# Performance work log

Measured on AMD Instinct MI355X. Metric: run time of the kernel, lower is better.

The kernel has to match this reference:

```python
import jax, jax.numpy as jnp
import numpy as np

B, S, D, H = 2, 2048, 1024, 16
DK = D // H


def setup_inputs() -> dict:
    key = jax.random.key(0)
    ks = jax.random.split(key, 12)
    sc = 1.0 / np.sqrt(D)
    inp = {
        'q': jax.random.normal(ks[0], (B, S, D), jnp.float32),
        'k': jax.random.normal(ks[1], (B, S, D), jnp.float32),
        'v': jax.random.normal(ks[2], (B, S, D), jnp.float32),
        'mask': jnp.tril(jnp.ones((S, S), jnp.int32))[None, None],  # causal [1,1,S,S]
        'w_q': jax.random.normal(ks[3], (D, D), jnp.float32) * sc,
        'b_q': jnp.zeros((D,), jnp.float32),
        'w_k': jax.random.normal(ks[4], (D, D), jnp.float32) * sc,
        'b_k': jnp.zeros((D,), jnp.float32),
        'w_v': jax.random.normal(ks[5], (D, D), jnp.float32) * sc,
        'b_v': jnp.zeros((D,), jnp.float32),
        'w_o': jax.random.normal(ks[6], (D, D), jnp.float32) * sc,
        'b_o': jnp.zeros((D,), jnp.float32),
    }
    return inp


def _split_heads(x):
    # [B,S,D] -> [B,H,S,DK]
    b, s, _ = x.shape
    return x.reshape(b, s, H, DK).transpose(0, 2, 1, 3)


def reference(q, k, v, mask, w_q, b_q, w_k, b_k, w_v, b_v, w_o, b_o):
    # Linear projections (torch Linear: x @ W.T + b)
    qh = _split_heads(q @ w_q.T + b_q)
    kh = _split_heads(k @ w_k.T + b_k)
    vh = _split_heads(v @ w_v.T + b_v)
    scores = jnp.einsum('bhqd,bhkd->bhqk', qh, kh) / jnp.sqrt(jnp.float32(DK))
    scores = jnp.where(mask == 0, jnp.float32(-1e9), scores)
    probs = jax.nn.softmax(scores, axis=-1)
    # dropout is identity in eval mode
    ctx = jnp.einsum('bhqk,bhkd->bhqd', probs, vh)  # [B,H,S,DK]
    ctx = ctx.transpose(0, 2, 1, 3).reshape(q.shape[0], -1, D)
    out = ctx @ w_o.T + b_o
    return out, probs
```

## Files before the change

### kernel.cpp

```cpp
#include <hip/hip_runtime.h>

typedef float f32x4 __attribute__((ext_vector_type(4)));
typedef short s16x8 __attribute__((ext_vector_type(8)));
typedef short s16x4 __attribute__((ext_vector_type(4)));

#define MFMA(a, b, c) __builtin_amdgcn_mfma_f32_16x16x32_bf16((a), (b), (c), 0, 0, 0)

static __device__ __forceinline__ short f2bf(float f) {
  union { float ff; unsigned u; } v; v.ff = f;
  unsigned r = v.u + 0x7FFFu + ((v.u >> 16) & 1u);
  return (short)(r >> 16);
}

typedef __attribute__((address_space(3))) void lds_void_t;
typedef const __attribute__((address_space(1))) void gmem_void_t;
static __device__ __forceinline__ void gload_lds16(const void* g, void* l) {
  __builtin_amdgcn_global_load_lds((gmem_void_t*)g, (lds_void_t*)l, 16, 0, 0);
}

__global__ __launch_bounds__(256) void cvt_qkv_kernel(
    const float* __restrict__ q, const float* __restrict__ k, const float* __restrict__ v,
    short* __restrict__ qo, short* __restrict__ ko, short* __restrict__ vo) {
  const int y = blockIdx.y;
  const float* s = (y == 0) ? q : (y == 1) ? k : v;
  short* d = (y == 0) ? qo : (y == 1) ? ko : vo;
  const int i = blockIdx.x * 256 + threadIdx.x;
  const f32x4* s4 = (const f32x4*)s;
  f32x4 a = s4[2 * i], b = s4[2 * i + 1];
  s16x8 o;
  o[0] = f2bf(a[0]); o[1] = f2bf(a[1]); o[2] = f2bf(a[2]); o[3] = f2bf(a[3]);
  o[4] = f2bf(b[0]); o[5] = f2bf(b[1]); o[6] = f2bf(b[2]); o[7] = f2bf(b[3]);
  ((s16x8*)d)[i] = o;
}

__global__ __launch_bounds__(256) void cvt_w_kernel(
    const float* __restrict__ w0, const float* __restrict__ w1,
    const float* __restrict__ w2, const float* __restrict__ w3,
    short* __restrict__ o0, short* __restrict__ o1,
    short* __restrict__ o2, short* __restrict__ o3) {
  const int y = blockIdx.y;
  const float* s = (y == 0) ? w0 : (y == 1) ? w1 : (y == 2) ? w2 : w3;
  short* d = (y == 0) ? o0 : (y == 1) ? o1 : (y == 2) ? o2 : o3;
  const int i = blockIdx.x * 256 + threadIdx.x;
  const f32x4* s4 = (const f32x4*)s;
  f32x4 a = s4[2 * i], b = s4[2 * i + 1];
  s16x8 o;
  o[0] = f2bf(a[0]); o[1] = f2bf(a[1]); o[2] = f2bf(a[2]); o[3] = f2bf(a[3]);
  o[4] = f2bf(b[0]); o[5] = f2bf(b[1]); o[6] = f2bf(b[2]); o[7] = f2bf(b[3]);
  ((s16x8*)d)[i] = o;
}

template <int MODE, int NFRAG>
static __device__ __forceinline__ void gemm_body(
    const short* __restrict__ A, const short* __restrict__ Bt,
    const float* __restrict__ bias, void* __restrict__ outp) {
  constexpr int BN = NFRAG * 32;
  __shared__ short As[4096];
  __shared__ short Bs[BN * 32];
  const int t = threadIdx.x;
  const int lane = t & 63, wave = t >> 6;
  const int wr = wave >> 1, wc = wave & 1;
  const int lr = lane & 15, lg = lane >> 4;
  const int mBase = blockIdx.x * 128, nBase = blockIdx.y * BN;

  const int rowA = t >> 2, kcA = (t & 3) << 3;
  const short* gA = A + (size_t)(mBase + rowA) * 1024 + kcA;
  const short* gB = Bt + (size_t)(nBase + rowA) * 1024 + kcA;

  f32x4 acc[4][NFRAG] = {};

  for (int k0 = 0; k0 < 1024; k0 += 32) {
    __syncthreads();
    gload_lds16(gA + k0, &As[t * 8]);
    gload_lds16(gA + 64 * 1024 + k0, &As[2048 + t * 8]);
    gload_lds16(gB + k0, &Bs[t * 8]);
    if constexpr (NFRAG == 4) gload_lds16(gB + 64 * 1024 + k0, &Bs[2048 + t * 8]);
    __syncthreads();
    const s16x8* Av = (const s16x8*)As;
    const s16x8* Bv = (const s16x8*)Bs;
    s16x8 af[4], bfr[NFRAG];
#pragma unroll
    for (int m = 0; m < 4; ++m) af[m] = Av[(wr * 64 + m * 16 + lr) * 4 + lg];
#pragma unroll
    for (int n = 0; n < NFRAG; ++n) bfr[n] = Bv[(wc * NFRAG * 16 + n * 16 + lr) * 4 + lg];
#pragma unroll
    for (int m = 0; m < 4; ++m)
#pragma unroll
      for (int n = 0; n < NFRAG; ++n)
        acc[m][n] = MFMA(af[m], bfr[n], acc[m][n]);
  }

  const int row0 = mBase + wr * 64 + lg * 4;
  const int col0 = nBase + wc * NFRAG * 16 + lr;
#pragma unroll
  for (int n = 0; n < NFRAG; ++n) {
    const int col = col0 + n * 16;
    const float bv = bias[col];
#pragma unroll
    for (int m = 0; m < 4; ++m) {
#pragma unroll
      for (int j = 0; j < 4; ++j) {
        const int r = row0 + m * 16 + j;
        const float val = acc[m][n][j] + bv;
        if (MODE == 0) {
          short* o = (short*)outp;
          const int bb = r >> 11, ss = r & 2047, hh = col >> 6, dd = col & 63;
          o[((size_t)(bb * 16 + hh) * 2048 + ss) * 64 + dd] = f2bf(val);
        } else {
          ((float*)outp)[(size_t)r * 1024 + col] = val;
        }
      }
    }
  }
}

__global__ __launch_bounds__(256) void gemm_qkv_kernel(
    const short* __restrict__ qb, const short* __restrict__ kb, const short* __restrict__ vb,
    const short* __restrict__ wqb, const short* __restrict__ wkb, const short* __restrict__ wvb,
    const float* __restrict__ bq, const float* __restrict__ bk, const float* __restrict__ bv,
    short* __restrict__ Qh, short* __restrict__ Kh, short* __restrict__ Vh) {
  const int z = blockIdx.z;
  const short* A  = (z == 0) ? qb : (z == 1) ? kb : vb;
  const short* Bt = (z == 0) ? wqb : (z == 1) ? wkb : wvb;
  const float* bias = (z == 0) ? bq : (z == 1) ? bk : bv;
  short* out = (z == 0) ? Qh : (z == 1) ? Kh : Vh;
  gemm_body<0, 4>(A, Bt, bias, out);
}

__global__ __launch_bounds__(256) void gemm_o_kernel(
    const short* __restrict__ A, const short* __restrict__ Bt,
    const float* __restrict__ bias, float* __restrict__ outp) {
  gemm_body<1, 2>(A, Bt, bias, outp);
}

__global__ __launch_bounds__(256) void attn_kernel(
    const short* __restrict__ Qh, const short* __restrict__ Kh,
    const short* __restrict__ Vh, float* __restrict__ probs,
    short* __restrict__ ctxo) {
  __shared__ short Ks[4096];
  __shared__ short Vt[4096];
  __shared__ short Pl[4096];
  const int t = threadIdx.x;
  const int lane = t & 63, w = t >> 6;
  const int lr = lane & 15, lg = lane >> 4;
  const int qblk = blockIdx.x, bh = blockIdx.y;
  const size_t hb = (size_t)bh * (2048 * 64);
  const int qBase = qblk * 64;

  const short* Kg = Kh + hb;
  const short* Vg = Vh + hb;

  const int qg = qBase + w * 16 + lr;
  const s16x8 qf0 = *(const s16x8*)(Qh + hb + (size_t)qg * 64 + lg * 8);
  const s16x8 qf1 = *(const s16x8*)(Qh + hb + (size_t)qg * 64 + 32 + lg * 8);

  const int vkey = lane;
  const int vdkb = w * 16;
  const int x = lr & 7;
  const int px = (lr & 7) << 3;

  float rs = 0.f;
  for (int kt = 0; kt <= qblk; ++kt) {
    const int kBase = kt * 64;
    __syncthreads();
    {
      int c = t, key = c >> 3, slot = c & 7;
      gload_lds16(Kg + (size_t)(kBase + key) * 64 + ((slot ^ (key & 7)) << 3), &Ks[c * 8]);
      c = t + 256; key = c >> 3; slot = c & 7;
      gload_lds16(Kg + (size_t)(kBase + key) * 64 + ((slot ^ (key & 7)) << 3), &Ks[c * 8]);
    }
    __syncthreads();
    const s16x8* Kv = (const s16x8*)Ks;
#pragma unroll
    for (int sub = 0; sub < 4; ++sub) {
      const int key = sub * 16 + lr;
      s16x8 kf0 = Kv[key * 8 + (lg ^ x)];
      s16x8 kf1 = Kv[key * 8 + ((lg + 4) ^ x)];
      f32x4 z = {0.f, 0.f, 0.f, 0.f};
      f32x4 sa = MFMA(kf0, qf0, z);
      sa = MFMA(kf1, qf1, sa);
      const int key0 = kBase + sub * 16 + lg * 4;
#pragma unroll
      for (int j = 0; j < 4; ++j)
        if (key0 + j <= qg) rs += __expf(sa[j] * 0.125f);
    }
  }
  rs += __shfl_xor(rs, 16);
  rs += __shfl_xor(rs, 32);
  const float rinv = 1.f / rs;

  f32x4 cacc[4] = {};
  for (int kt = 0; kt < 32; ++kt) {
    const int kBase = kt * 64;
    if (kt <= qblk) {
      __syncthreads();
      {
        int c = t, key = c >> 3, slot = c & 7;
        gload_lds16(Kg + (size_t)(kBase + key) * 64 + ((slot ^ (key & 7)) << 3), &Ks[c * 8]);
        c = t + 256; key = c >> 3; slot = c & 7;
        gload_lds16(Kg + (size_t)(kBase + key) * 64 + ((slot ^ (key & 7)) << 3), &Ks[c * 8]);
      }
      const s16x8* vsrc = (const s16x8*)(Vg + (size_t)(kBase + vkey) * 64 + vdkb);
      const s16x8 v0 = vsrc[0], v1 = vsrc[1];
#pragma unroll
      for (int i = 0; i < 8; ++i) {
        const int r0 = vdkb + i, r1 = vdkb + 8 + i;
        Vt[r0 * 64 + (vkey ^ ((r0 & 7) << 3))] = v0[i];
        Vt[r1 * 64 + (vkey ^ ((r1 & 7) << 3))] = v1[i];
      }
      __syncthreads();
      const s16x8* Kv = (const s16x8*)Ks;
#pragma unroll
      for (int sub = 0; sub < 4; ++sub) {
        const int key = sub * 16 + lr;
        s16x8 kf0 = Kv[key * 8 + (lg ^ x)];
        s16x8 kf1 = Kv[key * 8 + ((lg + 4) ^ x)];
        f32x4 z = {0.f, 0.f, 0.f, 0.f};
        f32x4 sa = MFMA(kf0, qf0, z);
        sa = MFMA(kf1, qf1, sa);
        const int key0 = kBase + sub * 16 + lg * 4;
        f32x4 p4;
#pragma unroll
        for (int j = 0; j < 4; ++j)
          p4[j] = (key0 + j <= qg) ? __expf(sa[j] * 0.125f) * rinv : 0.f;
        *(f32x4*)&probs[(size_t)(bh * 2048 + qg) * 2048 + key0] = p4;
        s16x4 pb;
        pb[0] = f2bf(p4[0]); pb[1] = f2bf(p4[1]);
        pb[2] = f2bf(p4[2]); pb[3] = f2bf(p4[3]);
        *(s16x4*)&Pl[w * 1024 + lr * 64 + ((sub * 16 + lg * 4) ^ px)] = pb;
      }
      const s16x8* Vv = (const s16x8*)Vt;
      const s16x8 pf0 = *(const s16x8*)&Pl[w * 1024 + lr * 64 + ((lg * 8) ^ px)];
      const s16x8 pf1 = *(const s16x8*)&Pl[w * 1024 + lr * 64 + ((32 + lg * 8) ^ px)];
#pragma unroll
      for (int n = 0; n < 4; ++n) {
        const int row = n * 16 + lr;
        s16x8 vf0 = Vv[row * 8 + (lg ^ x)];
        s16x8 vf1 = Vv[row * 8 + ((lg + 4) ^ x)];
        cacc[n] = MFMA(pf0, vf0, cacc[n]);
        cacc[n] = MFMA(pf1, vf1, cacc[n]);
      }
    } else {
      const f32x4 zz = {0.f, 0.f, 0.f, 0.f};
#pragma unroll
      for (int i = 0; i < 4; ++i) {
        const int row = qBase + w * 16 + i * 4 + lg;
        *(f32x4*)&probs[(size_t)(bh * 2048 + row) * 2048 + kBase + lr * 4] = zz;
      }
    }
  }

  const int bb = bh >> 4, hh = bh & 15;
#pragma unroll
  for (int n = 0; n < 4; ++n) {
    const int dcol = hh * 64 + n * 16 + lr;
#pragma unroll
    for (int j = 0; j < 4; ++j) {
      const int srow = qBase + w * 16 + lg * 4 + j;
      ctxo[(size_t)(bb * 2048 + srow) * 1024 + dcol] = f2bf(cacc[n][j]);
    }
  }
}

extern "C" void kernel_launch(void* const* d_in, const int* in_sizes, int n_in,
                              void* d_out, int out_size, void* d_ws, size_t ws_size,
                              hipStream_t stream) {
  const float* q  = (const float*)d_in[0];
  const float* k  = (const float*)d_in[1];
  const float* v  = (const float*)d_in[2];
  const float* wq = (const float*)d_in[4];
  const float* bq = (const float*)d_in[5];
  const float* wk = (const float*)d_in[6];
  const float* bk = (const float*)d_in[7];
  const float* wv = (const float*)d_in[8];
  const float* bv = (const float*)d_in[9];
  const float* wo = (const float*)d_in[10];
  const float* bo = (const float*)d_in[11];

  char* ws = (char*)d_ws;
  const size_t MB = 1u << 20;
  short* qb  = (short*)(ws);
  short* kb  = (short*)(ws + 8 * MB);
  short* vb  = (short*)(ws + 16 * MB);
  short* wqb = (short*)(ws + 24 * MB);
  short* wkb = (short*)(ws + 26 * MB);
  short* wvb = (short*)(ws + 28 * MB);
  short* wob = (short*)(ws + 30 * MB);
  short* Qh  = (short*)(ws + 32 * MB);
  short* Kh  = (short*)(ws + 40 * MB);
  short* Vh  = (short*)(ws + 48 * MB);
  short* ctx = (short*)(ws + 56 * MB);

  float* outp  = (float*)d_out;
  float* probs = outp + (size_t)4096 * 1024;

  cvt_qkv_kernel<<<dim3(2048, 3), 256, 0, stream>>>(q, k, v, qb, kb, vb);
  cvt_w_kernel<<<dim3(512, 4), 256, 0, stream>>>(wq, wk, wv, wo, wqb, wkb, wvb, wob);

  gemm_qkv_kernel<<<dim3(32, 8, 3), 256, 0, stream>>>(
      qb, kb, vb, wqb, wkb, wvb, bq, bk, bv, Qh, Kh, Vh);

  attn_kernel<<<dim3(32, 32), 256, 0, stream>>>(Qh, Kh, Vh, probs, ctx);

  gemm_o_kernel<<<dim3(32, 16), 256, 0, stream>>>(ctx, wob, bo, outp);
}
```

Baseline: 768.5 us.

## Double-buffer K/V tiles in attention and reverse query-block order

The attention kernel now double-buffers its K and V LDS tiles, so the next tile's loads are issued while the current tile is computed, and it drops to one barrier per iteration. Query blocks run in reverse order so the longest causal rows are scheduled first. The causal mask check is skipped on tiles that lie entirely below the diagonal. The zero upper-triangle region of probs is written in one up-front loop instead of inside the key loop. This doubles the K/V LDS footprint, which could reduce occupancy.

```diff
diff --git a/kernel.cpp b/kernel.cpp
--- a/kernel.cpp
+++ b/kernel.cpp
@@ -137,13 +137,14 @@
     const short* __restrict__ Qh, const short* __restrict__ Kh,
     const short* __restrict__ Vh, float* __restrict__ probs,
     short* __restrict__ ctxo) {
-  __shared__ short Ks[4096];
-  __shared__ short Vt[4096];
+  __shared__ short Ks[2][4096];
+  __shared__ short Vt[2][4096];
   __shared__ short Pl[4096];
   const int t = threadIdx.x;
   const int lane = t & 63, w = t >> 6;
   const int lr = lane & 15, lg = lane >> 4;
-  const int qblk = blockIdx.x, bh = blockIdx.y;
+  const int qblk = 31 - blockIdx.x;
+  const int bh = blockIdx.y;
   const size_t hb = (size_t)bh * (2048 * 64);
   const int qBase = qblk * 64;
 
@@ -154,23 +155,31 @@
   const s16x8 qf0 = *(const s16x8*)(Qh + hb + (size_t)qg * 64 + lg * 8);
   const s16x8 qf1 = *(const s16x8*)(Qh + hb + (size_t)qg * 64 + 32 + lg * 8);
 
-  const int vkey = lane;
-  const int vdkb = w * 16;
   const int x = lr & 7;
   const int px = (lr & 7) << 3;
 
+  {
+    const f32x4 zz = {0.f, 0.f, 0.f, 0.f};
+    float* prow = probs + (size_t)(bh * 2048 + qBase + w * 16 + lr) * 2048;
+    for (int c = qBase + 64 + lg * 4; c < 2048; c += 16)
+      *(f32x4*)&prow[c] = zz;
+  }
+
+  auto stageK = [&](int buf, int kt) {
+    const int kBase = kt * 64;
+    int c = t, key = c >> 3, slot = c & 7;
+    gload_lds16(Kg + (size_t)(kBase + key) * 64 + ((slot ^ (key & 7)) << 3), &Ks[buf][c * 8]);
+    c = t + 256; key = c >> 3; slot = c & 7;
+    gload_lds16(Kg + (size_t)(kBase + key) * 64 + ((slot ^ (key & 7)) << 3), &Ks[buf][c * 8]);
+  };
+
   float rs = 0.f;
+  stageK(0, 0);
+  __syncthreads();
   for (int kt = 0; kt <= qblk; ++kt) {
-    const int kBase = kt * 64;
-    __syncthreads();
-    {
-      int c = t, key = c >> 3, slot = c & 7;
-      gload_lds16(Kg + (size_t)(kBase + key) * 64 + ((slot ^ (key & 7)) << 3), &Ks[c * 8]);
-      c = t + 256; key = c >> 3; slot = c & 7;
-      gload_lds16(Kg + (size_t)(kBase + key) * 64 + ((slot ^ (key & 7)) << 3), &Ks[c * 8]);
-    }
-    __syncthreads();
-    const s16x8* Kv = (const s16x8*)Ks;
+    const int cur = kt & 1;
+    if (kt < qblk) stageK(cur ^ 1, kt + 1);
+    const s16x8* Kv = (const s16x8*)Ks[cur];
 #pragma unroll
     for (int sub = 0; sub < 4; ++sub) {
       const int key = sub * 16 + lr;
@@ -179,75 +188,87 @@
       f32x4 z = {0.f, 0.f, 0.f, 0.f};
       f32x4 sa = MFMA(kf0, qf0, z);
       sa = MFMA(kf1, qf1, sa);
-      const int key0 = kBase + sub * 16 + lg * 4;
-#pragma unroll
-      for (int j = 0; j < 4; ++j)
-        if (key0 + j <= qg) rs += __expf(sa[j] * 0.125f);
-    }
+      if (kt < qblk) {
+#pragma unroll
+        for (int j = 0; j < 4; ++j) rs += __expf(sa[j] * 0.125f);
+      } else {
+        const int key0 = kt * 64 + sub * 16 + lg * 4;
+#pragma unroll
+        for (int j = 0; j < 4; ++j)
+          if (key0 + j <= qg) rs += __expf(sa[j] * 0.125f);
+      }
+    }
+    __syncthreads();
   }
   rs += __shfl_xor(rs, 16);
   rs += __shfl_xor(rs, 32);
   const float rinv = 1.f / rs;
 
+  const int vkey = lane, vdkb = w * 16;
+  auto loadV = [&](int kt, s16x8& v0, s16x8& v1) {
+    const s16x8* vsrc = (const s16x8*)(Vg + (size_t)(kt * 64 + vkey) * 64 + vdkb);
+    v0 = vsrc[0]; v1 = vsrc[1];
+  };
+  auto writeV = [&](int buf, const s16x8& v0, const s16x8& v1) {
+#pragma unroll
+    for (int i = 0; i < 8; ++i) {
+      const int r0 = vdkb + i, r1 = vdkb + 8 + i;
+      Vt[buf][r0 * 64 + (vkey ^ ((r0 & 7) << 3))] = v0[i];
+      Vt[buf][r1 * 64 + (vkey ^ ((r1 & 7) << 3))] = v1[i];
+    }
+  };
+
   f32x4 cacc[4] = {};
-  for (int kt = 0; kt < 32; ++kt) {
-    const int kBase = kt * 64;
-    if (kt <= qblk) {
-      __syncthreads();
-      {
-        int c = t, key = c >> 3, slot = c & 7;
-        gload_lds16(Kg + (size_t)(kBase + key) * 64 + ((slot ^ (key & 7)) << 3), &Ks[c * 8]);
-        c = t + 256; key = c >> 3; slot = c & 7;
-        gload_lds16(Kg + (size_t)(kBase + key) * 64 + ((slot ^ (key & 7)) << 3), &Ks[c * 8]);
-      }
-      const s16x8* vsrc = (const s16x8*)(Vg + (size_t)(kBase + vkey) * 64 + vdkb);
-      const s16x8 v0 = vsrc[0], v1 = vsrc[1];
-#pragma unroll
-      for (int i = 0; i < 8; ++i) {
-        const int r0 = vdkb + i, r1 = vdkb + 8 + i;
-        Vt[r0 * 64 + (vkey ^ ((r0 & 7) << 3))] = v0[i];
-        Vt[r1 * 64 + (vkey ^ ((r1 & 7) << 3))] = v1[i];
-      }
-      __syncthreads();
-      const s16x8* Kv = (const s16x8*)Ks;
-#pragma unroll
-      for (int sub = 0; sub < 4; ++sub) {
-        const int key = sub * 16 + lr;
-        s16x8 kf0 = Kv[key * 8 + (lg ^ x)];
-        s16x8 kf1 = Kv[key * 8 + ((lg + 4) ^ x)];
-        f32x4 z = {0.f, 0.f, 0.f, 0.f};
-        f32x4 sa = MFMA(kf0, qf0, z);
-        sa = MFMA(kf1, qf1, sa);
-        const int key0 = kBase + sub * 16 + lg * 4;
-        f32x4 p4;
+  {
+    s16x8 v0, v1;
+    stageK(0, 0);
+    loadV(0, v0, v1);
+    writeV(0, v0, v1);
+    __syncthreads();
+  }
+  for (int kt = 0; kt <= qblk; ++kt) {
+    const int cur = kt & 1;
+    const bool pf = (kt < qblk);
+    s16x8 nv0, nv1;
+    if (pf) { stageK(cur ^ 1, kt + 1); loadV(kt + 1, nv0, nv1); }
+    const s16x8* Kv = (const s16x8*)Ks[cur];
+#pragma unroll
+    for (int sub = 0; sub < 4; ++sub) {
+      const int key = sub * 16 + lr;
+      s16x8 kf0 = Kv[key * 8 + (lg ^ x)];
+      s16x8 kf1 = Kv[key * 8 + ((lg + 4) ^ x)];
+      f32x4 z = {0.f, 0.f, 0.f, 0.f};
+      f32x4 sa = MFMA(kf0, qf0, z);
+      sa = MFMA(kf1, qf1, sa);
+      const int key0 = kt * 64 + sub * 16 + lg * 4;
+      f32x4 p4;
+      if (kt < qblk) {
+#pragma unroll
+        for (int j = 0; j < 4; ++j) p4[j] = __expf(sa[j] * 0.125f) * rinv;
+      } else {
 #pragma unroll
         for (int j = 0; j < 4; ++j)
           p4[j] = (key0 + j <= qg) ? __expf(sa[j] * 0.125f) * rinv : 0.f;
-        *(f32x4*)&probs[(size_t)(bh * 2048 + qg) * 2048 + key0] = p4;
-        s16x4 pb;
-        pb[0] = f2bf(p4[0]); pb[1] = f2bf(p4[1]);
-        pb[2] = f2bf(p4[2]); pb[3] = f2bf(p4[3]);
-        *(s16x4*)&Pl[w * 1024 + lr * 64 + ((sub * 16 + lg * 4) ^ px)] = pb;
       }
-      const s16x8* Vv = (const s16x8*)Vt;
-      const s16x8 pf0 = *(const s16x8*)&Pl[w * 1024 + lr * 64 + ((lg * 8) ^ px)];
-      const s16x8 pf1 = *(const s16x8*)&Pl[w * 1024 + lr * 64 + ((32 + lg * 8) ^ px)];
-#pragma unroll
-      for (int n = 0; n < 4; ++n) {
-        const int row = n * 16 + lr;
-        s16x8 vf0 = Vv[row * 8 + (lg ^ x)];
-        s16x8 vf1 = Vv[row * 8 + ((lg + 4) ^ x)];
-        cacc[n] = MFMA(pf0, vf0, cacc[n]);
-        cacc[n] = MFMA(pf1, vf1, cacc[n]);
-      }
-    } else {
-      const f32x4 zz = {0.f, 0.f, 0.f, 0.f};
-#pragma unroll
-      for (int i = 0; i < 4; ++i) {
-        const int row = qBase + w * 16 + i * 4 + lg;
-        *(f32x4*)&probs[(size_t)(bh * 2048 + row) * 2048 + kBase + lr * 4] = zz;
-      }
-    }
+      *(f32x4*)&probs[(size_t)(bh * 2048 + qg) * 2048 + key0] = p4;
+      s16x4 pb;
+      pb[0] = f2bf(p4[0]); pb[1] = f2bf(p4[1]);
+      pb[2] = f2bf(p4[2]); pb[3] = f2bf(p4[3]);
+      *(s16x4*)&Pl[w * 1024 + lr * 64 + ((sub * 16 + lg * 4) ^ px)] = pb;
+    }
+    if (pf) writeV(cur ^ 1, nv0, nv1);
+    const s16x8* Vv = (const s16x8*)Vt[cur];
+    const s16x8 pfa = *(const s16x8*)&Pl[w * 1024 + lr * 64 + ((lg * 8) ^ px)];
+    const s16x8 pfb = *(const s16x8*)&Pl[w * 1024 + lr * 64 + ((32 + lg * 8) ^ px)];
+#pragma unroll
+    for (int n = 0; n < 4; ++n) {
+      const int row = n * 16 + lr;
+      s16x8 vf0 = Vv[row * 8 + (lg ^ x)];
+      s16x8 vf1 = Vv[row * 8 + ((lg + 4) ^ x)];
+      cacc[n] = MFMA(pfa, vf0, cacc[n]);
+      cacc[n] = MFMA(pfb, vf1, cacc[n]);
+    }
+    __syncthreads();
   }
 
   const int bb = bh >> 4, hh = bh & 15;
```

Measured after the change: 777.0 us. About the same (+1.1%).
